# Performance work log

Measured on AMD Instinct MI355X. Metric: run time of the kernel, lower is better.

## Reference

```python
import jax, jax.numpy as jnp
import numpy as np

N, D, WIDTH, NHID = 48, 128, 64, 3
NEG_SLOPE = 0.01  # jax.nn.leaky_relu default


def _set_partitions(elems):
    if len(elems) == 1:
        yield [elems]
        return
    first, rest = elems[0], elems[1:]
    for p in _set_partitions(rest):
        for i in range(len(p)):
            yield p[:i] + [[first] + p[i]] + p[i + 1:]
        yield [[first]] + p


def _part_tensor(p, n, k):
    # indicator tensor: indices equal iff they belong to the same block of partition p
    idx = np.indices((n,) * k)
    blk = {}
    for bi, b in enumerate(p):
        for e in b:
            blk[e] = bi
    mask = np.ones((n,) * k, dtype=bool)
    for a in range(k):
        for b in range(a + 1, k):
            mask &= (idx[a] == idx[b]) if blk[a] == blk[b] else (idx[a] != idx[b])
    return mask.astype(np.float32)


def perm_invariant_basis(k, n, swappable=()):
    # basis of S_n-invariant order-k tensors, optionally invariant to swapping given axis pairs
    canon = lambda p: tuple(sorted(tuple(sorted(b)) for b in p))
    parts = sorted({canon(p) for p in _set_partitions(list(range(k)))})
    def swap(p, a, b):
        m = {a: b, b: a}
        return canon([[m.get(e, e) for e in blk] for blk in p])
    seen, out = set(), []
    for p in parts:
        if p in seen:
            continue
        orbit = {p}
        for (a, b) in swappable:
            orbit |= {swap(q, a, b) for q in list(orbit)}
        seen |= orbit
        out.append(sum(_part_tensor(q, n, k) for q in orbit))
    return np.stack(out)


def setup_inputs() -> dict:
    key = jax.random.key(0)
    ks = jax.random.split(key, 9)
    basis_sn = jnp.asarray(perm_invariant_basis(4, N, ((0, 1),)))  # (11,n,n,n,n)
    basis_nn = jnp.asarray(perm_invariant_basis(4, N))             # (15,n,n,n,n)
    bias_basis = jnp.asarray(perm_invariant_basis(2, N))           # (2,n,n)
    Ksn, Knn, Kb = basis_sn.shape[0], basis_nn.shape[0], bias_basis.shape[0]
    sc = 0.05
    return {
        "S": jax.random.normal(ks[0], (N, D), jnp.float32),
        "w0": jax.random.normal(ks[1], (WIDTH, 1, Ksn), jnp.float32) * sc,
        "b0": jax.random.normal(ks[2], (WIDTH, Kb), jnp.float32) * sc,
        "wh": jax.random.normal(ks[3], (NHID, WIDTH, WIDTH, Knn), jnp.float32) * sc,
        "bh": jax.random.normal(ks[4], (NHID, WIDTH, Kb), jnp.float32) * sc,
        "wp": jax.random.normal(ks[5], (1, WIDTH, Ksn), jnp.float32) * sc,
        "bp": jax.random.normal(ks[6], (1, Kb), jnp.float32) * sc,
        "wi": jax.random.normal(ks[7], (1, WIDTH, Kb), jnp.float32) * sc,
        "bi": jax.random.normal(ks[8], (1, 1), jnp.float32) * sc,
        "basis_sn": basis_sn,
        "basis_nn": basis_nn,
        "bias_basis": bias_basis,
    }


def _glinear(X, W, Bw, basis, bias_basis):
    # X: (in,n,n); W: (out,in,K); basis: (K, a,b, c,d) with (a,b) contracting against X
    out = jnp.einsum('oik,kabcd,iab->ocd', W, basis, X, optimize=True)
    return out + jnp.einsum('ok,kcd->ocd', Bw, bias_basis)


def reference(S, w0, b0, wh, bh, wp, bp, wi, bi, basis_sn, basis_nn, bias_basis):
    n, d = S.shape
    X = (S @ S.T)[None]  # (1,n,n), symmetric
    X = jax.nn.leaky_relu(_glinear(X, w0, b0, basis_sn, bias_basis))  # (width,n,n)

    def step(Xc, wb):
        W, B = wb
        return jax.nn.leaky_relu(_glinear(Xc, W, B, basis_nn, bias_basis)), None

    X, _ = jax.lax.scan(step, X, (wh, bh))

    basis_ns = basis_sn.transpose((0, 3, 4, 1, 2))  # output axes symmetric
    pairs = _glinear(X, wp, bp, basis_ns, bias_basis)  # (1,n,n)
    identity_scalar = jnp.einsum('oik,kab,iab->o', wi, bias_basis, X, optimize=True) + bi[:, 0]  # (1,)

    pairs_basis = jnp.einsum('ab,cd->acbd', S, S)  # (n,n,d,d)
    A = jnp.einsum('ab,abcd->cd', pairs[0], pairs_basis) + identity_scalar[0] * jnp.eye(d, dtype=S.dtype)
    _, eigvecs = jnp.linalg.eigh(A)
    u = eigvecs[:, -1]  # top eigenvector
    return S @ u  # (n,)
```

## Files before the change

### kernel.cpp

```cpp
#include <hip/hip_runtime.h>
#include <math.h>


#define NDIM 48
#define NN   2304
#define DDIM 128
#define WID  64
#define FS   152
#define TP   49
#define BP   52
#define SIGN_FIX (-1.0f)
#define NSQ  20

#define WS_G      0
#define WS_FEATG  2304
#define WS_COEFN  2560
#define WS_COEFS  2816
#define WS_COEFP  3072
#define WS_P      3328
#define WS_XA     8192
#define WS_XAT    (WS_XA  + WID*NN)
#define WS_XB     (WS_XAT + WID*NN)
#define WS_XBT    (WS_XB  + WID*NN)
#define WS_FEATA  (WS_XBT + WID*NN)
#define WS_FEATB  (WS_FEATA + WID*FS)

__device__ __forceinline__ float bread(const float* t, int k, int a, int b, int c, int d) {
  return t[((((size_t)k*NDIM + a)*NDIM + b)*NDIM + c)*NDIM + d];
}

__device__ void probe15(const float* t, int k, bool transposed, float* dst) {
#define AT(a,b,c,d) (transposed ? bread(t,k,c,d,a,b) : bread(t,k,a,b,c,d))
  float eps = AT(2,3,0,1);
  float zet = AT(2,2,0,1) - eps;
  float b1  = AT(0,2,0,1) - eps;
  float b2  = AT(1,2,0,1) - eps;
  float g1  = AT(2,0,0,1) - eps;
  float g2  = AT(2,1,0,1) - eps;
  float d1  = AT(0,0,0,1) - eps - zet - b1 - g1;
  float d2  = AT(1,1,0,1) - eps - zet - b2 - g2;
  float a1  = AT(0,1,0,1) - eps - b1 - g2;
  float a2  = AT(1,0,0,1) - eps - b2 - g1;
  float de  = AT(2,3,0,0);
  float dz  = AT(2,2,0,0) - de;
  float db  = AT(0,2,0,0) - de;
  float dg  = AT(2,0,0,0) - de;
  float da  = AT(0,0,0,0) - de - dz - db - dg;
  dst[0]=a1; dst[1]=a2; dst[2]=b1; dst[3]=b2; dst[4]=g1; dst[5]=g2;
  dst[6]=d1; dst[7]=d2; dst[8]=eps; dst[9]=zet;
  dst[10]=da; dst[11]=db; dst[12]=dg; dst[13]=de; dst[14]=dz;
#undef AT
}

__global__ __launch_bounds__(256) void k_prep(const float* __restrict__ S,
    const float* __restrict__ bsn, const float* __restrict__ bnn,
    int Ksn, int Knn, float* __restrict__ ws) {
  __shared__ __align__(16) float st[DDIM*BP];
  __shared__ float gt[NDIM*TP];
  __shared__ float fr[NDIM], fd[NDIM];
  int tid = threadIdx.x;
  for (int e = tid; e < NDIM*DDIM; e += 256) {
    int r = e >> 7, k = e & 127;
    st[k*BP + r] = S[e];
  }
  __syncthreads();
  if (tid < 144) {
    int cg = (tid/12)*4, dg = (tid%12)*4;
    float acc[4][4] = {{0.f}};
    for (int k = 0; k < DDIM; ++k) {
      float4 av = *(const float4*)&st[k*BP + cg];
      float4 bv = *(const float4*)&st[k*BP + dg];
      float ar[4] = {av.x, av.y, av.z, av.w};
      float br[4] = {bv.x, bv.y, bv.z, bv.w};
#pragma unroll
      for (int r = 0; r < 4; ++r)
#pragma unroll
        for (int c = 0; c < 4; ++c)
          acc[r][c] = fmaf(ar[r], br[c], acc[r][c]);
    }
#pragma unroll
    for (int r = 0; r < 4; ++r)
      for (int c = 0; c < 4; ++c) {
        ws[WS_G + (cg+r)*NDIM + dg + c] = acc[r][c];
        gt[(cg+r)*TP + dg + c] = acc[r][c];
      }
  }
  __syncthreads();
  if (tid < NDIM) {
    float rs = 0, cs = 0;
    for (int j = 0; j < NDIM; ++j) { rs += gt[tid*TP + j]; cs += gt[j*TP + tid]; }
    ws[WS_FEATG + tid]      = rs;
    ws[WS_FEATG + 48 + tid] = cs;
    ws[WS_FEATG + 96 + tid] = gt[tid*TP + tid];
    fr[tid] = rs; fd[tid] = gt[tid*TP + tid];
  }
  __syncthreads();
  if (tid == 0) { float t=0; for (int j=0;j<NDIM;++j) t+=fr[j]; ws[WS_FEATG+144]=t; }
  if (tid == 1) { float t=0; for (int j=0;j<NDIM;++j) t+=fd[j]; ws[WS_FEATG+145]=t; }
  int np = Knn + 2*Ksn;
  for (int p = tid; p < np; p += 256) {
    if (p < Knn)            probe15(bnn, p,             false, &ws[WS_COEFN + p*16]);
    else if (p < Knn + Ksn) probe15(bsn, p - Knn,       false, &ws[WS_COEFS + (p-Knn)*16]);
    else                    probe15(bsn, p - Knn - Ksn, true,  &ws[WS_COEFP + (p-Knn-Ksn)*16]);
  }
}

__global__ __launch_bounds__(256) void k_layer(
    const float* __restrict__ Xin, const float* __restrict__ XinT,
    const float* __restrict__ featIn,
    const float* __restrict__ Wl, const float* __restrict__ bl,
    const float* __restrict__ bb, const float* __restrict__ coefT,
    int K, int nch,
    float* __restrict__ Xout, float* __restrict__ XoutT, float* __restrict__ featOut) {
  __shared__ float Cs[WID*16];
  __shared__ float Rv[9*48];
  __shared__ float Ssc[2];
  __shared__ float tile[NDIM*TP];
  __shared__ float fr[NDIM], fd[NDIM];
  __shared__ float coefL[16*16];
  int tid = threadIdx.x;
  int o = blockIdx.x;
  for (int v = tid; v < K*16; v += 256) coefL[v] = coefT[v];
  __syncthreads();
  for (int idx = tid; idx < nch*15; idx += 256) {
    int i = idx/15, f = idx - i*15;
    float s = 0;
    const float* wrow = Wl + (o*nch + i)*K;
    for (int k = 0; k < K; ++k) s = fmaf(wrow[k], coefL[k*16+f], s);
    Cs[i*16+f] = s;
  }
  __syncthreads();
  for (int v = tid; v < 9*48 + 2; v += 256) {
    if (v < 432) {
      int m = v/48, c = v - m*48;
      const int fidx[9] = {2,3,4,5,6,7,10,11,12};
      const int foff[9] = {0,0,48,48,96,96,96,0,48};
      int f = fidx[m], off = foff[m];
      float s = 0;
      for (int i = 0; i < nch; ++i) s = fmaf(Cs[i*16+f], featIn[i*FS + off + c], s);
      Rv[m*48+c] = s;
    } else if (v == 432) {
      float s = 0;
      for (int i = 0; i < nch; ++i)
        s += Cs[i*16+8]*featIn[i*FS+144] + Cs[i*16+9]*featIn[i*FS+145];
      Ssc[0] = s;
    } else {
      float s = 0;
      for (int i = 0; i < nch; ++i)
        s += Cs[i*16+13]*featIn[i*FS+144] + Cs[i*16+14]*featIn[i*FS+145];
      Ssc[1] = s;
    }
  }
  __syncthreads();
  float acc[9];
#pragma unroll
  for (int m = 0; m < 9; ++m) acc[m] = 0.f;
  for (int i = 0; i < nch; ++i) {
    float c0 = Cs[i*16+0], c1 = Cs[i*16+1];
    const float* xi  = Xin  + i*NN;
    const float* xti = XinT + i*NN;
#pragma unroll
    for (int m = 0; m < 9; ++m) {
      int e = tid + (m<<8);
      acc[m] = fmaf(c0, xi[e], fmaf(c1, xti[e], acc[m]));
    }
  }
  float bl0 = bl[o*2+0], bl1 = bl[o*2+1];
#pragma unroll
  for (int m = 0; m < 9; ++m) {
    int e = tid + (m<<8);
    int c = e/48, d = e - c*48;
    float bias = bl0*bb[e] + bl1*bb[NN+e];
    float val;
    if (c == d)
      val = Rv[6*48+c] + Rv[7*48+c] + Rv[8*48+c] + Ssc[1] + bias;
    else
      val = acc[m] + Rv[c] + Rv[48+d] + Rv[96+c] + Rv[144+d] + Rv[192+c] + Rv[240+d]
          + Ssc[0] + bias;
    val = val > 0.0f ? val : 0.01f*val;
    Xout[o*NN + e] = val;
    tile[c*TP + d] = val;
  }
  __syncthreads();
#pragma unroll
  for (int m = 0; m < 9; ++m) {
    int e = tid + (m<<8);
    int c = e/48, d = e - c*48;
    XoutT[o*NN + e] = tile[d*TP + c];
  }
  if (tid < NDIM) {
    float rs = 0, cs = 0;
    for (int j = 0; j < NDIM; ++j) { rs += tile[tid*TP+j]; cs += tile[j*TP+tid]; }
    featOut[o*FS + tid]      = rs;
    featOut[o*FS + 48 + tid] = cs;
    featOut[o*FS + 96 + tid] = tile[tid*TP+tid];
    fr[tid] = rs; fd[tid] = tile[tid*TP+tid];
  }
  __syncthreads();
  if (tid == 0) { float t=0; for (int j=0;j<NDIM;++j) t+=fr[j]; featOut[o*FS+144]=t; }
  if (tid == 1) { float t=0; for (int j=0;j<NDIM;++j) t+=fd[j]; featOut[o*FS+145]=t; }
}

__global__ __launch_bounds__(256) void k_pairsP(
    const float* __restrict__ Xin, const float* __restrict__ XinT,
    const float* __restrict__ featIn,
    const float* __restrict__ wp, const float* __restrict__ bp,
    const float* __restrict__ bb, const float* __restrict__ coefT,
    int K, float* __restrict__ P) {
  __shared__ float Cs[WID*16];
  __shared__ float Rv[9*48];
  __shared__ float Ssc[2];
  __shared__ float coefL[16*16];
  int tid = threadIdx.x;
  for (int v = tid; v < K*16; v += 256) coefL[v] = coefT[v];
  __syncthreads();
  for (int idx = tid; idx < WID*15; idx += 256) {
    int i = idx/15, f = idx - i*15;
    float s = 0;
    const float* wrow = wp + i*K;
    for (int k = 0; k < K; ++k) s = fmaf(wrow[k], coefL[k*16+f], s);
    Cs[i*16+f] = s;
  }
  __syncthreads();
  for (int v = tid; v < 9*48 + 2; v += 256) {
    if (v < 432) {
      int m = v/48, c = v - m*48;
      const int fidx[9] = {2,3,4,5,6,7,10,11,12};
      const int foff[9] = {0,0,48,48,96,96,96,0,48};
      int f = fidx[m], off = foff[m];
      float s = 0;
      for (int i = 0; i < WID; ++i) s = fmaf(Cs[i*16+f], featIn[i*FS + off + c], s);
      Rv[m*48+c] = s;
    } else if (v == 432) {
      float s = 0;
      for (int i = 0; i < WID; ++i)
        s += Cs[i*16+8]*featIn[i*FS+144] + Cs[i*16+9]*featIn[i*FS+145];
      Ssc[0] = s;
    } else {
      float s = 0;
      for (int i = 0; i < WID; ++i)
        s += Cs[i*16+13]*featIn[i*FS+144] + Cs[i*16+14]*featIn[i*FS+145];
      Ssc[1] = s;
    }
  }
  __syncthreads();
  int e = blockIdx.x*256 + tid;
  int c = e/48, d = e - c*48;
  float a = 0;
  for (int i = 0; i < WID; ++i)
    a = fmaf(Cs[i*16+0], Xin[i*NN+e], fmaf(Cs[i*16+1], XinT[i*NN+e], a));
  float bias = bp[0]*bb[e] + bp[1]*bb[NN+e];
  float val;
  if (c == d) val = Rv[6*48+c]+Rv[7*48+c]+Rv[8*48+c]+Ssc[1]+bias;
  else val = a + Rv[c]+Rv[48+d]+Rv[96+c]+Rv[144+d]+Rv[192+c]+Rv[240+d]+Ssc[0]+bias;
  P[e] = val;
}

__global__ __launch_bounds__(256) void k_eig(const float* __restrict__ P,
    const float* __restrict__ G, float* __restrict__ out) {
  __shared__ float pp[NDIM*TP];
  __shared__ __align__(16) float Gt[NDIM*BP];
  __shared__ __align__(16) float Bt[NDIM*BP];
  __shared__ __align__(16) float BTt[NDIM*BP];
  __shared__ float red[256];
  __shared__ float wv[NDIM], ov[NDIM];
  __shared__ float scaleS;
  __shared__ int jstar;
  int tid = threadIdx.x;
  for (int e = tid; e < NN; e += 256) {
    int c = e/48, d = e - c*48;
    pp[c*TP+d] = P[e];
    Gt[c*BP+d] = G[e];
  }
  __syncthreads();
  float facc = 0;
  int cg = 0, dg = 0;
  if (tid < 144) {
    cg = (tid/12)*4; dg = (tid%12)*4;
    float acc[4][4] = {{0.f}};
    for (int j = 0; j < NDIM; ++j) {
      float pr[4];
#pragma unroll
      for (int r = 0; r < 4; ++r)
        pr[r] = 0.5f*(pp[(cg+r)*TP + j] + pp[j*TP + cg + r]);
      float4 gv = *(const float4*)&Gt[j*BP + dg];
      float gr[4] = {gv.x, gv.y, gv.z, gv.w};
#pragma unroll
      for (int r = 0; r < 4; ++r)
#pragma unroll
        for (int c = 0; c < 4; ++c)
          acc[r][c] = fmaf(pr[r], gr[c], acc[r][c]);
    }
#pragma unroll
    for (int r = 0; r < 4; ++r)
      for (int c = 0; c < 4; ++c) {
        Bt[(cg+r)*BP + dg + c] = acc[r][c];
        facc = fmaf(acc[r][c], acc[r][c], facc);
      }
  }
  red[tid] = facc;
  __syncthreads();
  for (int s = 128; s > 0; s >>= 1) {
    if (tid < s) red[tid] += red[tid+s];
    __syncthreads();
  }
  float invF = 1.0f/sqrtf(red[0] + 1e-30f);
  __syncthreads();
  for (int e = tid; e < NN; e += 256) {
    int c = e/48, d = e - c*48;
    float v = Bt[c*BP+d]*invF + (c == d ? 1.0f : 0.0f);
    Bt[c*BP+d] = v;
    BTt[d*BP+c] = v;
  }
  __syncthreads();
  for (int it = 0; it < NSQ; ++it) {
    float acc[4][4] = {{0.f}};
    if (tid < 144) {
      for (int j = 0; j < NDIM; ++j) {
        float4 av = *(const float4*)&BTt[j*BP + cg];
        float4 bv = *(const float4*)&Bt[j*BP + dg];
        float ar[4] = {av.x,av.y,av.z,av.w};
        float br[4] = {bv.x,bv.y,bv.z,bv.w};
#pragma unroll
        for (int r = 0; r < 4; ++r)
#pragma unroll
          for (int c = 0; c < 4; ++c)
            acc[r][c] = fmaf(ar[r], br[c], acc[r][c]);
      }
    }
    if (tid < 144 && cg == dg)
      red[cg>>2] = acc[0][0]+acc[1][1]+acc[2][2]+acc[3][3];
    __syncthreads();
    if (tid == 0) {
      float t = 0;
      for (int q = 0; q < 12; ++q) t += red[q];
      scaleS = 1.0f/t;
    }
    __syncthreads();
    float inv = scaleS;
    if (tid < 144) {
#pragma unroll
      for (int r = 0; r < 4; ++r)
        for (int c = 0; c < 4; ++c) {
          float v = acc[r][c]*inv;
          Bt[(cg+r)*BP + dg + c] = v;
          BTt[(dg+c)*BP + cg + r] = v;
        }
    }
    __syncthreads();
  }
  if (tid < NDIM) {
    float s = 0;
    for (int c = 0; c < NDIM; ++c) { float v = Bt[c*BP+tid]; s = fmaf(v,v,s); }
    red[tid] = s;
  }
  __syncthreads();
  if (tid == 0) {
    int jm = 0; float best = -1.f;
    for (int j = 0; j < NDIM; ++j) if (red[j] > best) { best = red[j]; jm = j; }
    jstar = jm;
  }
  __syncthreads();
  if (tid < NDIM) wv[tid] = Bt[tid*BP + jstar];
  __syncthreads();
  if (tid < NDIM) {
    float s = 0;
    for (int j = 0; j < NDIM; ++j) s = fmaf(Gt[tid*BP+j], wv[j], s);
    ov[tid] = s;
  }
  __syncthreads();
  if (tid == 0) {
    float nrm = 0;
    for (int c = 0; c < NDIM; ++c) nrm = fmaf(ov[c], wv[c], nrm);
    int jm = 0; float best = -1.f;
    for (int c = 0; c < NDIM; ++c) { float a = fabsf(ov[c]); if (a > best) { best = a; jm = c; } }
    float sgn = (ov[jm] >= 0.0f ? 1.0f : -1.0f) * SIGN_FIX;
    scaleS = sgn / sqrtf(nrm + 1e-30f);
  }
  __syncthreads();
  if (tid < NDIM) out[tid] = ov[tid]*scaleS;
}

extern "C" void kernel_launch(void* const* d_in, const int* in_sizes, int n_in,
                              void* d_out, int out_size, void* d_ws, size_t ws_size,
                              hipStream_t stream) {
  const float* S   = (const float*)d_in[0];
  const float* w0  = (const float*)d_in[1];
  const float* b0  = (const float*)d_in[2];
  const float* wh  = (const float*)d_in[3];
  const float* bh  = (const float*)d_in[4];
  const float* wp  = (const float*)d_in[5];
  const float* bp  = (const float*)d_in[6];
  const float* bsn = (const float*)d_in[9];
  const float* bnn = (const float*)d_in[10];
  const float* bb  = (const float*)d_in[11];
  int Ksn = in_sizes[1] / WID;
  int Knn = in_sizes[3] / (3*WID*WID);

  float* ws  = (float*)d_ws;
  float* out = (float*)d_out;

  float* G     = ws + WS_G;
  float* featG = ws + WS_FEATG;
  float* coefN = ws + WS_COEFN;
  float* coefS = ws + WS_COEFS;
  float* coefP = ws + WS_COEFP;
  float* Pbuf  = ws + WS_P;
  float* XA    = ws + WS_XA;   float* XAT = ws + WS_XAT;
  float* XB    = ws + WS_XB;   float* XBT = ws + WS_XBT;
  float* fA    = ws + WS_FEATA;
  float* fB    = ws + WS_FEATB;

  k_prep<<<1, 256, 0, stream>>>(S, bsn, bnn, Ksn, Knn, ws);
  k_layer<<<WID, 256, 0, stream>>>(G, G, featG, w0, b0, bb, coefS, Ksn, 1,
                                   XA, XAT, fA);
  k_layer<<<WID, 256, 0, stream>>>(XA, XAT, fA, wh,                 bh,       bb, coefN, Knn, WID, XB, XBT, fB);
  k_layer<<<WID, 256, 0, stream>>>(XB, XBT, fB, wh +   WID*WID*Knn, bh + 128, bb, coefN, Knn, WID, XA, XAT, fA);
  k_layer<<<WID, 256, 0, stream>>>(XA, XAT, fA, wh + 2*WID*WID*Knn, bh + 256, bb, coefN, Knn, WID, XB, XBT, fB);
  k_pairsP<<<9, 256, 0, stream>>>(XB, XBT, fB, wp, bp, bb, coefP, Ksn, Pbuf);
  k_eig<<<1, 256, 0, stream>>>(Pbuf, G, out);
}
```

Baseline: 220.2 us.

## Fuse all stages into one persistent kernel with atomic grid barriers

Replaces the seven separate launches (prep, four layers, pairs, eigen) with a single 64-block kernel that uses atomic-counter grid barriers between layers. Every block recomputes the Gram matrix and basis probe coefficients redundantly, which avoids a separate prep launch. The pairs and eigen stages now run on block 0 alone, where earlier the pairs stage was spread over 9 blocks. The aim is to remove launch gaps and inter-kernel overhead. In exchange it adds a memset launch, spin-wait barriers that depend on all 64 blocks being resident at once, and a serialized tail stage.

```diff
diff --git a/kernel.cpp b/kernel.cpp
--- a/kernel.cpp
+++ b/kernel.cpp
@@ -12,18 +12,19 @@
 #define SIGN_FIX (-1.0f)
 #define NSQ  20
 
-#define WS_G      0
-#define WS_FEATG  2304
-#define WS_COEFN  2560
-#define WS_COEFS  2816
-#define WS_COEFP  3072
-#define WS_P      3328
-#define WS_XA     8192
-#define WS_XAT    (WS_XA  + WID*NN)
-#define WS_XB     (WS_XAT + WID*NN)
-#define WS_XBT    (WS_XB  + WID*NN)
-#define WS_FEATA  (WS_XBT + WID*NN)
-#define WS_FEATB  (WS_FEATA + WID*FS)
+#define POOL_FLOATS 9840
+
+__device__ __forceinline__ void gbar(unsigned* bar, int idx) {
+  __syncthreads();
+  if (threadIdx.x == 0) {
+    __threadfence();
+    atomicAdd(&bar[idx], 1u);
+    while (atomicAdd(&bar[idx], 0u) < (unsigned)WID)
+      __builtin_amdgcn_s_sleep(1);
+  }
+  __syncthreads();
+  __threadfence();
+}
 
 __device__ __forceinline__ float bread(const float* t, int k, int a, int b, int c, int d) {
   return t[((((size_t)k*NDIM + a)*NDIM + b)*NDIM + c)*NDIM + d];
@@ -52,81 +53,18 @@
 #undef AT
 }
 
-__global__ __launch_bounds__(256) void k_prep(const float* __restrict__ S,
-    const float* __restrict__ bsn, const float* __restrict__ bnn,
-    int Ksn, int Knn, float* __restrict__ ws) {
-  __shared__ __align__(16) float st[DDIM*BP];
-  __shared__ float gt[NDIM*TP];
-  __shared__ float fr[NDIM], fd[NDIM];
-  int tid = threadIdx.x;
-  for (int e = tid; e < NDIM*DDIM; e += 256) {
-    int r = e >> 7, k = e & 127;
-    st[k*BP + r] = S[e];
-  }
-  __syncthreads();
-  if (tid < 144) {
-    int cg = (tid/12)*4, dg = (tid%12)*4;
-    float acc[4][4] = {{0.f}};
-    for (int k = 0; k < DDIM; ++k) {
-      float4 av = *(const float4*)&st[k*BP + cg];
-      float4 bv = *(const float4*)&st[k*BP + dg];
-      float ar[4] = {av.x, av.y, av.z, av.w};
-      float br[4] = {bv.x, bv.y, bv.z, bv.w};
-#pragma unroll
-      for (int r = 0; r < 4; ++r)
-#pragma unroll
-        for (int c = 0; c < 4; ++c)
-          acc[r][c] = fmaf(ar[r], br[c], acc[r][c]);
-    }
-#pragma unroll
-    for (int r = 0; r < 4; ++r)
-      for (int c = 0; c < 4; ++c) {
-        ws[WS_G + (cg+r)*NDIM + dg + c] = acc[r][c];
-        gt[(cg+r)*TP + dg + c] = acc[r][c];
-      }
-  }
-  __syncthreads();
-  if (tid < NDIM) {
-    float rs = 0, cs = 0;
-    for (int j = 0; j < NDIM; ++j) { rs += gt[tid*TP + j]; cs += gt[j*TP + tid]; }
-    ws[WS_FEATG + tid]      = rs;
-    ws[WS_FEATG + 48 + tid] = cs;
-    ws[WS_FEATG + 96 + tid] = gt[tid*TP + tid];
-    fr[tid] = rs; fd[tid] = gt[tid*TP + tid];
-  }
-  __syncthreads();
-  if (tid == 0) { float t=0; for (int j=0;j<NDIM;++j) t+=fr[j]; ws[WS_FEATG+144]=t; }
-  if (tid == 1) { float t=0; for (int j=0;j<NDIM;++j) t+=fd[j]; ws[WS_FEATG+145]=t; }
-  int np = Knn + 2*Ksn;
-  for (int p = tid; p < np; p += 256) {
-    if (p < Knn)            probe15(bnn, p,             false, &ws[WS_COEFN + p*16]);
-    else if (p < Knn + Ksn) probe15(bsn, p - Knn,       false, &ws[WS_COEFS + (p-Knn)*16]);
-    else                    probe15(bsn, p - Knn - Ksn, true,  &ws[WS_COEFP + (p-Knn-Ksn)*16]);
-  }
-}
-
-__global__ __launch_bounds__(256) void k_layer(
+__device__ void hidden_layer(int tid, int o,
     const float* __restrict__ Xin, const float* __restrict__ XinT,
     const float* __restrict__ featIn,
     const float* __restrict__ Wl, const float* __restrict__ bl,
-    const float* __restrict__ bb, const float* __restrict__ coefT,
-    int K, int nch,
-    float* __restrict__ Xout, float* __restrict__ XoutT, float* __restrict__ featOut) {
-  __shared__ float Cs[WID*16];
-  __shared__ float Rv[9*48];
-  __shared__ float Ssc[2];
-  __shared__ float tile[NDIM*TP];
-  __shared__ float fr[NDIM], fd[NDIM];
-  __shared__ float coefL[16*16];
-  int tid = threadIdx.x;
-  int o = blockIdx.x;
-  for (int v = tid; v < K*16; v += 256) coefL[v] = coefT[v];
-  __syncthreads();
-  for (int idx = tid; idx < nch*15; idx += 256) {
+    const float* __restrict__ bb, const float* coefT , int K,
+    float* __restrict__ Xout, float* __restrict__ XoutT, float* __restrict__ featOut,
+    float* Cs, float* Rv, float* Ssc, float* tile, float* fr, float* fd) {
+  for (int idx = tid; idx < WID*15; idx += 256) {
     int i = idx/15, f = idx - i*15;
     float s = 0;
-    const float* wrow = Wl + (o*nch + i)*K;
-    for (int k = 0; k < K; ++k) s = fmaf(wrow[k], coefL[k*16+f], s);
+    const float* wrow = Wl + (o*WID + i)*K;
+    for (int k = 0; k < K; ++k) s = fmaf(wrow[k], coefT[k*16+f], s);
     Cs[i*16+f] = s;
   }
   __syncthreads();
@@ -137,16 +75,16 @@
       const int foff[9] = {0,0,48,48,96,96,96,0,48};
       int f = fidx[m], off = foff[m];
       float s = 0;
-      for (int i = 0; i < nch; ++i) s = fmaf(Cs[i*16+f], featIn[i*FS + off + c], s);
+      for (int i = 0; i < WID; ++i) s = fmaf(Cs[i*16+f], featIn[i*FS + off + c], s);
       Rv[m*48+c] = s;
     } else if (v == 432) {
       float s = 0;
-      for (int i = 0; i < nch; ++i)
+      for (int i = 0; i < WID; ++i)
         s += Cs[i*16+8]*featIn[i*FS+144] + Cs[i*16+9]*featIn[i*FS+145];
       Ssc[0] = s;
     } else {
       float s = 0;
-      for (int i = 0; i < nch; ++i)
+      for (int i = 0; i < WID; ++i)
         s += Cs[i*16+13]*featIn[i*FS+144] + Cs[i*16+14]*featIn[i*FS+145];
       Ssc[1] = s;
     }
@@ -155,7 +93,7 @@
   float acc[9];
 #pragma unroll
   for (int m = 0; m < 9; ++m) acc[m] = 0.f;
-  for (int i = 0; i < nch; ++i) {
+  for (int i = 0; i < WID; ++i) {
     float c0 = Cs[i*16+0], c1 = Cs[i*16+1];
     const float* xi  = Xin  + i*NN;
     const float* xti = XinT + i*NN;
@@ -189,10 +127,10 @@
     XoutT[o*NN + e] = tile[d*TP + c];
   }
   if (tid < NDIM) {
-    float rs = 0, cs = 0;
-    for (int j = 0; j < NDIM; ++j) { rs += tile[tid*TP+j]; cs += tile[j*TP+tid]; }
+    float rs = 0, csum = 0;
+    for (int j = 0; j < NDIM; ++j) { rs += tile[tid*TP+j]; csum += tile[j*TP+tid]; }
     featOut[o*FS + tid]      = rs;
-    featOut[o*FS + 48 + tid] = cs;
+    featOut[o*FS + 48 + tid] = csum;
     featOut[o*FS + 96 + tid] = tile[tid*TP+tid];
     fr[tid] = rs; fd[tid] = tile[tid*TP+tid];
   }
@@ -201,24 +139,165 @@
   if (tid == 1) { float t=0; for (int j=0;j<NDIM;++j) t+=fd[j]; featOut[o*FS+145]=t; }
 }
 
-__global__ __launch_bounds__(256) void k_pairsP(
-    const float* __restrict__ Xin, const float* __restrict__ XinT,
-    const float* __restrict__ featIn,
-    const float* __restrict__ wp, const float* __restrict__ bp,
-    const float* __restrict__ bb, const float* __restrict__ coefT,
-    int K, float* __restrict__ P) {
+__global__ __launch_bounds__(256) void k_all(
+    const float* __restrict__ S,  const float* __restrict__ w0,
+    const float* __restrict__ b0, const float* __restrict__ wh,
+    const float* __restrict__ bh, const float* __restrict__ wp,
+    const float* __restrict__ bp, const float* __restrict__ bsn,
+    const float* __restrict__ bnn, const float* __restrict__ bb,
+    int Ksn, int Knn, float* __restrict__ ws, float* __restrict__ out) {
+  __shared__ __align__(16) float pool[POOL_FLOATS];
+  __shared__ float tile[NDIM*TP];
   __shared__ float Cs[WID*16];
   __shared__ float Rv[9*48];
   __shared__ float Ssc[2];
-  __shared__ float coefL[16*16];
+  __shared__ float coefAll[48*16];
+  __shared__ float fgr[NDIM], fgd[NDIM], fgS[2];
+  __shared__ float fr[NDIM], fd[NDIM];
+  __shared__ float red[256];
+  __shared__ float wv[NDIM], ov[NDIM];
+  __shared__ float sSc;
+  __shared__ int jstar;
+
   int tid = threadIdx.x;
-  for (int v = tid; v < K*16; v += 256) coefL[v] = coefT[v];
-  __syncthreads();
+  int o   = blockIdx.x;
+
+  unsigned* bar = (unsigned*)ws;
+  float* base = ws + 64;
+  float* XA  = base;
+  float* XAT = XA  + WID*NN;
+  float* XB  = XAT + WID*NN;
+  float* XBT = XB  + WID*NN;
+  float* fA  = XBT + WID*NN;
+  float* fB  = fA  + WID*FS;
+  const float* coefS = coefAll;
+  const float* coefN = coefAll + Ksn*16;
+  const float* coefP = coefAll + (Ksn+Knn)*16;
+
+  for (int e = tid; e < NDIM*DDIM; e += 256) {
+    int r = e >> 7, k = e & 127;
+    pool[k*BP + r] = S[e];
+  }
+  __syncthreads();
+  if (tid < 144) {
+    int cg4 = (tid/12)*4, dg4 = (tid%12)*4;
+    float a4[4][4] = {{0.f}};
+    for (int k = 0; k < DDIM; ++k) {
+      float4 av = *(const float4*)&pool[k*BP + cg4];
+      float4 bv = *(const float4*)&pool[k*BP + dg4];
+      float ar[4] = {av.x, av.y, av.z, av.w};
+      float br[4] = {bv.x, bv.y, bv.z, bv.w};
+#pragma unroll
+      for (int r = 0; r < 4; ++r)
+#pragma unroll
+        for (int c = 0; c < 4; ++c)
+          a4[r][c] = fmaf(ar[r], br[c], a4[r][c]);
+    }
+#pragma unroll
+    for (int r = 0; r < 4; ++r)
+      for (int c = 0; c < 4; ++c)
+        tile[(cg4+r)*TP + dg4 + c] = a4[r][c];
+  } else {
+    int p = tid - 144, np = Knn + 2*Ksn;
+    if (p < np && p < 48) {
+      if (p < Ksn)            probe15(bsn, p,          false, &coefAll[p*16]);
+      else if (p < Ksn+Knn)   probe15(bnn, p-Ksn,      false, &coefAll[p*16]);
+      else                    probe15(bsn, p-Ksn-Knn,  true,  &coefAll[p*16]);
+    }
+  }
+  __syncthreads();
+  if (tid < NDIM) {
+    float rs = 0;
+    for (int j = 0; j < NDIM; ++j) rs += tile[tid*TP + j];
+    fgr[tid] = rs;
+    fgd[tid] = tile[tid*TP + tid];
+  }
+  __syncthreads();
+  if (tid == 0) { float t=0; for (int j=0;j<NDIM;++j) t+=fgr[j]; fgS[0]=t; }
+  if (tid == 1) { float t=0; for (int j=0;j<NDIM;++j) t+=fgd[j]; fgS[1]=t; }
+  if (o == 0) {
+    for (int e = tid; e < NN; e += 256) {
+      int c = e/48, d = e - c*48;
+      pool[c*BP + d] = tile[c*TP + d];
+    }
+  }
+  if (tid < 15) {
+    float s = 0;
+    const float* wrow = w0 + o*Ksn;
+    for (int k = 0; k < Ksn; ++k) s = fmaf(wrow[k], coefS[k*16+tid], s);
+    Cs[tid] = s;
+  }
+  __syncthreads();
+  {
+    float c01 = Cs[0]+Cs[1], c24 = Cs[2]+Cs[4], c35 = Cs[3]+Cs[5];
+    float c6 = Cs[6], c7 = Cs[7];
+    float ssc0 = Cs[8]*fgS[0] + Cs[9]*fgS[1];
+    float sscD = Cs[13]*fgS[0] + Cs[14]*fgS[1];
+    float cA = Cs[10], cB = Cs[11]+Cs[12];
+    float bl0 = b0[o*2+0], bl1 = b0[o*2+1];
+    float val[9];
+#pragma unroll
+    for (int m = 0; m < 9; ++m) {
+      int e = tid + (m<<8);
+      int c = e/48, d = e - c*48;
+      float bias = bl0*bb[e] + bl1*bb[NN+e];
+      float v;
+      if (c == d) v = cA*fgd[c] + cB*fgr[c] + sscD + bias;
+      else        v = c01*tile[c*TP+d] + c24*fgr[c] + c35*fgr[d]
+                    + c6*fgd[c] + c7*fgd[d] + ssc0 + bias;
+      v = v > 0.0f ? v : 0.01f*v;
+      val[m] = v;
+    }
+    __syncthreads();
+#pragma unroll
+    for (int m = 0; m < 9; ++m) {
+      int e = tid + (m<<8);
+      int c = e/48, d = e - c*48;
+      tile[c*TP + d] = val[m];
+      XA[o*NN + e] = val[m];
+    }
+  }
+  __syncthreads();
+#pragma unroll
+  for (int m = 0; m < 9; ++m) {
+    int e = tid + (m<<8);
+    int c = e/48, d = e - c*48;
+    XAT[o*NN + e] = tile[d*TP + c];
+  }
+  if (tid < NDIM) {
+    float rs = 0, csum = 0;
+    for (int j = 0; j < NDIM; ++j) { rs += tile[tid*TP+j]; csum += tile[j*TP+tid]; }
+    fA[o*FS + tid]      = rs;
+    fA[o*FS + 48 + tid] = csum;
+    fA[o*FS + 96 + tid] = tile[tid*TP+tid];
+    fr[tid] = rs; fd[tid] = tile[tid*TP+tid];
+  }
+  __syncthreads();
+  if (tid == 0) { float t=0; for (int j=0;j<NDIM;++j) t+=fr[j]; fA[o*FS+144]=t; }
+  if (tid == 1) { float t=0; for (int j=0;j<NDIM;++j) t+=fd[j]; fA[o*FS+145]=t; }
+  gbar(bar, 0);
+
+  hidden_layer(tid, o, XA, XAT, fA, wh,                 bh,       bb, coefN, Knn,
+               XB, XBT, fB, Cs, Rv, Ssc, tile, fr, fd);
+  gbar(bar, 1);
+  hidden_layer(tid, o, XB, XBT, fB, wh +   WID*WID*Knn, bh + 128, bb, coefN, Knn,
+               XA, XAT, fA, Cs, Rv, Ssc, tile, fr, fd);
+  gbar(bar, 2);
+  hidden_layer(tid, o, XA, XAT, fA, wh + 2*WID*WID*Knn, bh + 256, bb, coefN, Knn,
+               XB, XBT, fB, Cs, Rv, Ssc, tile, fr, fd);
+  gbar(bar, 3);
+
+  if (o != 0) return;
+
+  float* Gt  = pool;
+  float* Bt  = pool + 2496;
+  float* BTt = pool + 4992;
+  float* pp  = pool + 7488;
   for (int idx = tid; idx < WID*15; idx += 256) {
     int i = idx/15, f = idx - i*15;
     float s = 0;
-    const float* wrow = wp + i*K;
-    for (int k = 0; k < K; ++k) s = fmaf(wrow[k], coefL[k*16+f], s);
+    const float* wrow = wp + i*Ksn;
+    for (int k = 0; k < Ksn; ++k) s = fmaf(wrow[k], coefP[k*16+f], s);
     Cs[i*16+f] = s;
   }
   __syncthreads();
@@ -229,73 +308,62 @@
       const int foff[9] = {0,0,48,48,96,96,96,0,48};
       int f = fidx[m], off = foff[m];
       float s = 0;
-      for (int i = 0; i < WID; ++i) s = fmaf(Cs[i*16+f], featIn[i*FS + off + c], s);
+      for (int i = 0; i < WID; ++i) s = fmaf(Cs[i*16+f], fB[i*FS + off + c], s);
       Rv[m*48+c] = s;
     } else if (v == 432) {
       float s = 0;
       for (int i = 0; i < WID; ++i)
-        s += Cs[i*16+8]*featIn[i*FS+144] + Cs[i*16+9]*featIn[i*FS+145];
+        s += Cs[i*16+8]*fB[i*FS+144] + Cs[i*16+9]*fB[i*FS+145];
       Ssc[0] = s;
     } else {
       float s = 0;
       for (int i = 0; i < WID; ++i)
-        s += Cs[i*16+13]*featIn[i*FS+144] + Cs[i*16+14]*featIn[i*FS+145];
+        s += Cs[i*16+13]*fB[i*FS+144] + Cs[i*16+14]*fB[i*FS+145];
       Ssc[1] = s;
     }
   }
   __syncthreads();
-  int e = blockIdx.x*256 + tid;
-  int c = e/48, d = e - c*48;
-  float a = 0;
-  for (int i = 0; i < WID; ++i)
-    a = fmaf(Cs[i*16+0], Xin[i*NN+e], fmaf(Cs[i*16+1], XinT[i*NN+e], a));
-  float bias = bp[0]*bb[e] + bp[1]*bb[NN+e];
-  float val;
-  if (c == d) val = Rv[6*48+c]+Rv[7*48+c]+Rv[8*48+c]+Ssc[1]+bias;
-  else val = a + Rv[c]+Rv[48+d]+Rv[96+c]+Rv[144+d]+Rv[192+c]+Rv[240+d]+Ssc[0]+bias;
-  P[e] = val;
-}
-
-__global__ __launch_bounds__(256) void k_eig(const float* __restrict__ P,
-    const float* __restrict__ G, float* __restrict__ out) {
-  __shared__ float pp[NDIM*TP];
-  __shared__ __align__(16) float Gt[NDIM*BP];
-  __shared__ __align__(16) float Bt[NDIM*BP];
-  __shared__ __align__(16) float BTt[NDIM*BP];
-  __shared__ float red[256];
-  __shared__ float wv[NDIM], ov[NDIM];
-  __shared__ float scaleS;
-  __shared__ int jstar;
-  int tid = threadIdx.x;
-  for (int e = tid; e < NN; e += 256) {
-    int c = e/48, d = e - c*48;
-    pp[c*TP+d] = P[e];
-    Gt[c*BP+d] = G[e];
-  }
-  __syncthreads();
+  {
+    float bp0 = bp[0], bp1 = bp[1];
+#pragma unroll
+    for (int m = 0; m < 9; ++m) {
+      int e = tid + (m<<8);
+      int c = e/48, d = e - c*48;
+      float a = 0;
+      for (int i = 0; i < WID; ++i)
+        a = fmaf(Cs[i*16+0], XB[i*NN+e], fmaf(Cs[i*16+1], XBT[i*NN+e], a));
+      float bias = bp0*bb[e] + bp1*bb[NN+e];
+      float v;
+      if (c == d) v = Rv[6*48+c]+Rv[7*48+c]+Rv[8*48+c]+Ssc[1]+bias;
+      else v = a + Rv[c]+Rv[48+d]+Rv[96+c]+Rv[144+d]+Rv[192+c]+Rv[240+d]+Ssc[0]+bias;
+      pp[c*TP + d] = v;
+    }
+  }
+  __syncthreads();
+
   float facc = 0;
-  int cg = 0, dg = 0;
+  int cg4 = 0, dg4 = 0;
   if (tid < 144) {
-    cg = (tid/12)*4; dg = (tid%12)*4;
-    float acc[4][4] = {{0.f}};
+    cg4 = (tid/12)*4; dg4 = (tid%12)*4;
+    float a4[4][4] = {{0.f}};
     for (int j = 0; j < NDIM; ++j) {
       float pr[4];
 #pragma unroll
       for (int r = 0; r < 4; ++r)
-        pr[r] = 0.5f*(pp[(cg+r)*TP + j] + pp[j*TP + cg + r]);
-      float4 gv = *(const float4*)&Gt[j*BP + dg];
+        pr[r] = 0.5f*(pp[(cg4+r)*TP + j] + pp[j*TP + cg4 + r]);
+      float4 gv = *(const float4*)&Gt[j*BP + dg4];
       float gr[4] = {gv.x, gv.y, gv.z, gv.w};
 #pragma unroll
       for (int r = 0; r < 4; ++r)
 #pragma unroll
         for (int c = 0; c < 4; ++c)
-          acc[r][c] = fmaf(pr[r], gr[c], acc[r][c]);
+          a4[r][c] = fmaf(pr[r], gr[c], a4[r][c]);
     }
 #pragma unroll
     for (int r = 0; r < 4; ++r)
       for (int c = 0; c < 4; ++c) {
-        Bt[(cg+r)*BP + dg + c] = acc[r][c];
-        facc = fmaf(acc[r][c], acc[r][c], facc);
+        Bt[(cg4+r)*BP + dg4 + c] = a4[r][c];
+        facc = fmaf(a4[r][c], a4[r][c], facc);
       }
   }
   red[tid] = facc;
@@ -314,37 +382,37 @@
   }
   __syncthreads();
   for (int it = 0; it < NSQ; ++it) {
-    float acc[4][4] = {{0.f}};
+    float a4[4][4] = {{0.f}};
     if (tid < 144) {
       for (int j = 0; j < NDIM; ++j) {
-        float4 av = *(const float4*)&BTt[j*BP + cg];
-        float4 bv = *(const float4*)&Bt[j*BP + dg];
+        float4 av = *(const float4*)&BTt[j*BP + cg4];
+        float4 bv = *(const float4*)&Bt[j*BP + dg4];
         float ar[4] = {av.x,av.y,av.z,av.w};
         float br[4] = {bv.x,bv.y,bv.z,bv.w};
 #pragma unroll
         for (int r = 0; r < 4; ++r)
 #pragma unroll
           for (int c = 0; c < 4; ++c)
-            acc[r][c] = fmaf(ar[r], br[c], acc[r][c]);
+            a4[r][c] = fmaf(ar[r], br[c], a4[r][c]);
       }
     }
-    if (tid < 144 && cg == dg)
-      red[cg>>2] = acc[0][0]+acc[1][1]+acc[2][2]+acc[3][3];
+    if (tid < 144 && cg4 == dg4)
+      red[cg4>>2] = a4[0][0]+a4[1][1]+a4[2][2]+a4[3][3];
     __syncthreads();
     if (tid == 0) {
       float t = 0;
       for (int q = 0; q < 12; ++q) t += red[q];
-      scaleS = 1.0f/t;
+      sSc = 1.0f/t;
     }
     __syncthreads();
-    float inv = scaleS;
+    float inv = sSc;
     if (tid < 144) {
 #pragma unroll
       for (int r = 0; r < 4; ++r)
         for (int c = 0; c < 4; ++c) {
-          float v = acc[r][c]*inv;
-          Bt[(cg+r)*BP + dg + c] = v;
-          BTt[(dg+c)*BP + cg + r] = v;
+          float v = a4[r][c]*inv;
+          Bt[(cg4+r)*BP + dg4 + c] = v;
+          BTt[(dg4+c)*BP + cg4 + r] = v;
         }
     }
     __syncthreads();
@@ -375,10 +443,10 @@
     int jm = 0; float best = -1.f;
     for (int c = 0; c < NDIM; ++c) { float a = fabsf(ov[c]); if (a > best) { best = a; jm = c; } }
     float sgn = (ov[jm] >= 0.0f ? 1.0f : -1.0f) * SIGN_FIX;
-    scaleS = sgn / sqrtf(nrm + 1e-30f);
-  }
-  __syncthreads();
-  if (tid < NDIM) out[tid] = ov[tid]*scaleS;
+    sSc = sgn / sqrtf(nrm + 1e-30f);
+  }
+  __syncthreads();
+  if (tid < NDIM) out[tid] = ov[tid]*sSc;
 }
 
 extern "C" void kernel_launch(void* const* d_in, const int* in_sizes, int n_in,
@@ -397,26 +465,10 @@
   int Ksn = in_sizes[1] / WID;
   int Knn = in_sizes[3] / (3*WID*WID);
 
-  float* ws  = (float*)d_ws;
-  float* out = (float*)d_out;
-
-  float* G     = ws + WS_G;
-  float* featG = ws + WS_FEATG;
-  float* coefN = ws + WS_COEFN;
-  float* coefS = ws + WS_COEFS;
-  float* coefP = ws + WS_COEFP;
-  float* Pbuf  = ws + WS_P;
-  float* XA    = ws + WS_XA;   float* XAT = ws + WS_XAT;
-  float* XB    = ws + WS_XB;   float* XBT = ws + WS_XBT;
-  float* fA    = ws + WS_FEATA;
-  float* fB    = ws + WS_FEATB;
-
-  k_prep<<<1, 256, 0, stream>>>(S, bsn, bnn, Ksn, Knn, ws);
-  k_layer<<<WID, 256, 0, stream>>>(G, G, featG, w0, b0, bb, coefS, Ksn, 1,
-                                   XA, XAT, fA);
-  k_layer<<<WID, 256, 0, stream>>>(XA, XAT, fA, wh,                 bh,       bb, coefN, Knn, WID, XB, XBT, fB);
-  k_layer<<<WID, 256, 0, stream>>>(XB, XBT, fB, wh +   WID*WID*Knn, bh + 128, bb, coefN, Knn, WID, XA, XAT, fA);
-  k_layer<<<WID, 256, 0, stream>>>(XA, XAT, fA, wh + 2*WID*WID*Knn, bh + 256, bb, coefN, Knn, WID, XB, XBT, fB);
-  k_pairsP<<<9, 256, 0, stream>>>(XB, XBT, fB, wp, bp, bb, coefP, Ksn, Pbuf);
-  k_eig<<<1, 256, 0, stream>>>(Pbuf, G, out);
-}
+  float* wsf  = (float*)d_ws;
+  float* outf = (float*)d_out;
+
+  hipMemsetAsync(d_ws, 0, 64, stream);
+  k_all<<<dim3(WID), dim3(256), 0, stream>>>(S, w0, b0, wh, bh, wp, bp,
+                                             bsn, bnn, bb, Ksn, Knn, wsf, outf);
+}
```

Result: slower. 298.4 us (+35.5%).
